# Kernel optimization log

Hardware: AMD Instinct MI355X
Metric: run time of the kernel (lower is better)

The kernel has to match this reference:

```python
import jax, jax.numpy as jnp
import numpy as np

H = 16      # n_head
DK = 64     # d_k = n_feat // n_head
EPS = 1e-5  # nn.LayerNorm default eps


def _layernorm(x, gamma, beta):
    # LayerNorm over the last (d_k) dim, matching nn.LayerNorm(d_k)
    mu = jnp.mean(x, axis=-1, keepdims=True)
    var = jnp.mean(jnp.square(x - mu), axis=-1, keepdims=True)
    return (x - mu) * jax.lax.rsqrt(var + EPS) * gamma + beta


def setup_inputs() -> dict:
    key = jax.random.key(0)
    ks = jax.random.split(key, 10)
    B, T, D = 4, 1024, 1024
    s = 0.02
    inp = {
        "query": jax.random.normal(ks[0], (B, T, D), dtype=jnp.float32),
        "key":   jax.random.normal(ks[1], (B, T, D), dtype=jnp.float32),
        "value": jax.random.normal(ks[2], (B, T, D), dtype=jnp.float32),
        "mask":  jax.random.randint(ks[3], (B, T, T), 0, 2).astype(bool),
        # projection weights (torch nn.Linear: y = x @ W.T + b)
        "Wq": jax.random.normal(ks[4], (D, D), dtype=jnp.float32) * s,
        "bq": jnp.zeros((D,), dtype=jnp.float32),
        "Wk": jax.random.normal(ks[5], (D, D), dtype=jnp.float32) * s,
        "bk": jnp.zeros((D,), dtype=jnp.float32),
        "Wv": jax.random.normal(ks[6], (D, D), dtype=jnp.float32) * s,
        "bv": jnp.zeros((D,), dtype=jnp.float32),
        "Wo": jax.random.normal(ks[7], (D, D), dtype=jnp.float32) * s,
        "bo": jnp.zeros((D,), dtype=jnp.float32),
        # per-head LayerNorm params over d_k
        "q_gamma": jnp.ones((DK,), dtype=jnp.float32),
        "q_beta":  jnp.zeros((DK,), dtype=jnp.float32),
        "k_gamma": jnp.ones((DK,), dtype=jnp.float32),
        "k_beta":  jnp.zeros((DK,), dtype=jnp.float32),
    }
    return inp


def reference(query, key, value, mask, Wq, bq, Wk, bk, Wv, bv, Wo, bo,
              q_gamma, q_beta, k_gamma, k_beta):
    B, Tq, D = query.shape
    Tk = key.shape[1]
    # forward_qkv: project, split heads, QK-LayerNorm
    q = (query @ Wq.T + bq).reshape(B, Tq, H, DK)
    k = (key   @ Wk.T + bk).reshape(B, Tk, H, DK)
    q = _layernorm(q, q_gamma, q_beta).transpose(0, 2, 1, 3)  # (B,H,Tq,dk)
    k = _layernorm(k, k_gamma, k_beta).transpose(0, 2, 1, 3)  # (B,H,Tk,dk)
    v = (value @ Wv.T + bv).reshape(B, Tk, H, DK).transpose(0, 2, 1, 3)
    # scores scaled by sqrt(d_k)
    scores = jnp.einsum('bhqd,bhkd->bhqk', q, k) / jnp.sqrt(jnp.float32(DK))
    m = mask[:, None]  # (B,1,Tq,Tk) broadcast over heads
    scores = jnp.where(m, jnp.float32(-10000.0), scores)
    attn = jax.nn.softmax(scores, axis=-1)
    attn = jnp.where(m, jnp.float32(0.0), attn)
    # dropout is identity (p=0.0, eval)
    x = jnp.einsum('bhqk,bhkd->bhqd', attn, v)
    x = x.transpose(0, 2, 1, 3).reshape(B, Tq, H * DK)
    return x @ Wo.T + bo
```

## Files before the change

### kernel.cpp

```cpp
#include <hip/hip_runtime.h>
#include <cstdint>
#include <cstddef>

typedef _Float16 half8  __attribute__((ext_vector_type(8)));
typedef _Float16 half4v __attribute__((ext_vector_type(4)));
typedef float    f32x4  __attribute__((ext_vector_type(4)));

__device__ __forceinline__ f32x4 fzero4() {
  f32x4 v; v[0] = v[1] = v[2] = v[3] = 0.0f; return v;
}

__device__ __forceinline__ void gload16(const void* g, void* l) {
  __builtin_amdgcn_global_load_lds(
      (const __attribute__((address_space(1))) unsigned int*)g,
      (__attribute__((address_space(3))) unsigned int*)l, 16, 0, 0);
}

#define MFMA(a, b, c) __builtin_amdgcn_mfma_f32_16x16x32_f16(a, b, c, 0, 0, 0)
#define EXP2(x) __builtin_amdgcn_exp2f(x)

__device__ __forceinline__ float row16_sum(float x) {
#define STEP_(N)                                                         \
  {                                                                      \
    int t_ = __builtin_amdgcn_update_dpp(0, __float_as_int(x), 0x120 | N, \
                                         0xf, 0xf, true);                \
    x = x + __int_as_float(t_);                                          \
  }
  STEP_(8) STEP_(4) STEP_(2) STEP_(1)
#undef STEP_
  return x;
}

struct PrepArgs {
  const float* src[7];
  _Float16*    dst[7];
  const int*   mask;
  unsigned long long* mbits;
};

__global__ __launch_bounds__(256) void prep_kernel(PrepArgs a) {
  const int z = blockIdx.y;
  const int nthr = gridDim.x * blockDim.x;
  const int t0 = blockIdx.x * blockDim.x + threadIdx.x;
  if (z < 3) {
    const float4* __restrict__ s = (const float4*)a.src[z];
    half4v* __restrict__ d = (half4v*)a.dst[z];
    float4 v[8];
#pragma unroll
    for (int k = 0; k < 8; ++k) v[k] = s[t0 + k * nthr];
#pragma unroll
    for (int k = 0; k < 8; ++k) {
      half4v h;
      h[0] = (_Float16)v[k].x; h[1] = (_Float16)v[k].y;
      h[2] = (_Float16)v[k].z; h[3] = (_Float16)v[k].w;
      d[t0 + k * nthr] = h;
    }
  } else if (z < 7) {
    const float4* __restrict__ s = (const float4*)a.src[z];
    half4v* __restrict__ d = (half4v*)a.dst[z];
    float4 v[2];
#pragma unroll
    for (int k = 0; k < 2; ++k) v[k] = s[t0 + k * nthr];
#pragma unroll
    for (int k = 0; k < 2; ++k) {
      half4v h;
      h[0] = (_Float16)v[k].x; h[1] = (_Float16)v[k].y;
      h[2] = (_Float16)v[k].z; h[3] = (_Float16)v[k].w;
      d[t0 + k * nthr] = h;
    }
  } else {
    const int* __restrict__ src = a.mask;
    const unsigned char* __restrict__ s8 = (const unsigned char*)src;
    unsigned long long* __restrict__ dst = a.mbits;
    const int lane = threadIdx.x & 63;
    unsigned probe = 0;
#pragma unroll
    for (int e = 0; e < 16; ++e) probe |= s8[4 * (lane * 16 + e) + 1];
    const bool isbool = __any(probe != 0);

    const int gw = blockIdx.x * 4 + (threadIdx.x >> 6);
    for (int ii = 0; ii < 32; ii += 8) {
      int mv[8];
#pragma unroll
      for (int k = 0; k < 8; ++k) {
        const int word = gw * 32 + ii + k;
        const int t = word & 1023;
        const int kw = (word >> 10) & 15;
        const int b = word >> 14;
        const size_t idx = ((size_t)(b * 1024 + t)) * 1024 + kw * 64 + lane;
        mv[k] = isbool ? (int)s8[idx] : src[idx];
      }
#pragma unroll
      for (int k = 0; k < 8; ++k) {
        unsigned long long bal = __ballot(mv[k] != 0);
        if (lane == 0) dst[gw * 32 + ii + k] = bal;
      }
    }
  }
}

#define SM_SCALE 0.18033688011112042f

__global__ __launch_bounds__(256) void proj_kernel(
    const _Float16* __restrict__ q16, const _Float16* __restrict__ k16,
    const _Float16* __restrict__ v16, const _Float16* __restrict__ w16,
    const float* __restrict__ bq, const float* __restrict__ bk,
    const float* __restrict__ bv,
    const float* __restrict__ qg, const float* __restrict__ qbt,
    const float* __restrict__ kg, const float* __restrict__ kbt,
    _Float16* __restrict__ Qln, _Float16* __restrict__ Kln,
    _Float16* __restrict__ VT) {
  __shared__ _Float16 As[2][128 * 64];
  __shared__ _Float16 Bs[2][128 * 64];

  const int tid = threadIdx.x;
  const int w = tid >> 6, lane = tid & 63, g = lane >> 4, l15 = lane & 15;
  const int flat = blockIdx.x;
  const int swz = (flat & 7) * 96 + (flat >> 3);
  const int bn = swz & 7;
  const int bm = (swz >> 3) & 31;
  const int z = swz >> 8;

  const _Float16* A = (z == 0) ? q16 : ((z == 1) ? k16 : v16);
  const _Float16* W = w16 + (size_t)z * (1024 * 1024);
  const float* bias = (z == 0) ? bq : ((z == 1) ? bk : bv);

  const int wr = w >> 1, wc = w & 1;
  const int srow = (w << 3) + (lane >> 3);
  const int csw = ((lane & 7) ^ (lane >> 3)) << 3;
  const int rsw = (l15 & 7) << 3;

  f32x4 acc[4][4];
#pragma unroll
  for (int i = 0; i < 4; ++i)
#pragma unroll
    for (int j = 0; j < 4; ++j) acc[i][j] = fzero4();

#define PROJ_STAGE(KT, BUF)                                                 \
  _Pragma("unroll") for (int r = 0; r < 4; ++r) {                           \
    const int row = r * 32 + srow;                                          \
    gload16(A + (size_t)(bm * 128 + row) * 1024 + (KT)*64 + csw,            \
            &As[BUF][(r * 32 + (w << 3)) * 64]);                            \
    gload16(W + (size_t)(bn * 128 + row) * 1024 + (KT)*64 + csw,            \
            &Bs[BUF][(r * 32 + (w << 3)) * 64]);                            \
  }

#define PROJ_TILE(KT, CUR, NXT, PF)                                         \
  {                                                                         \
    if (PF) { PROJ_STAGE((KT) + 1, NXT) }                                   \
    _Pragma("unroll") for (int kk = 0; kk < 2; ++kk) {                      \
      half8 a[4], b[4];                                                     \
      _Pragma("unroll") for (int mi = 0; mi < 4; ++mi) a[mi] =              \
          *(const half8*)&As[CUR][(wr * 64 + mi * 16 + l15) * 64 +          \
                                  ((kk * 32 + g * 8) ^ rsw)];               \
      _Pragma("unroll") for (int nj = 0; nj < 4; ++nj) b[nj] =              \
          *(const half8*)&Bs[CUR][(wc * 64 + nj * 16 + l15) * 64 +          \
                                  ((kk * 32 + g * 8) ^ rsw)];               \
      __builtin_amdgcn_s_setprio(1);                                        \
      _Pragma("unroll") for (int mi = 0; mi < 4; ++mi)                      \
          _Pragma("unroll") for (int nj = 0; nj < 4; ++nj) acc[mi][nj] =    \
              MFMA(a[mi], b[nj], acc[mi][nj]);                              \
      __builtin_amdgcn_s_setprio(0);                                        \
    }                                                                       \
    if (PF) {                                                               \
      asm volatile("s_waitcnt vmcnt(0)" ::: "memory");                      \
      __syncthreads();                                                      \
    }                                                                       \
  }

  PROJ_STAGE(0, 0)
  asm volatile("s_waitcnt vmcnt(0)" ::: "memory");
  __syncthreads();
  for (int kt = 0; kt < 16; kt += 2) {
    PROJ_TILE(kt, 0, 1, true);
    PROJ_TILE(kt + 1, 1, 0, (kt + 1) < 15);
  }
#undef PROJ_TILE
#undef PROJ_STAGE

  const int colbase = bn * 128 + wc * 64;
  const int h = colbase >> 6;
  const int rowbase = bm * 128 + wr * 64;

  float biasv[4];
#pragma unroll
  for (int nj = 0; nj < 4; ++nj) biasv[nj] = bias[colbase + nj * 16 + l15];

  if (z < 2) {
    const float* gamma = (z == 0) ? qg : kg;
    const float* beta = (z == 0) ? qbt : kbt;
    const float sc = (z == 0) ? SM_SCALE : 1.0f;
    _Float16* dst = (z == 0) ? Qln : Kln;
    float gam[4], bet[4];
#pragma unroll
    for (int nj = 0; nj < 4; ++nj) {
      gam[nj] = gamma[nj * 16 + l15] * sc;
      bet[nj] = beta[nj * 16 + l15] * sc;
    }
#pragma unroll
    for (int mi = 0; mi < 4; ++mi) {
#pragma unroll
      for (int j = 0; j < 4; ++j) {
        float vals[4], s = 0.f, s2 = 0.f;
#pragma unroll
        for (int nj = 0; nj < 4; ++nj) {
          float v = acc[mi][nj][j] + biasv[nj];
          vals[nj] = v; s += v; s2 += v * v;
        }
        s = row16_sum(s);
        s2 = row16_sum(s2);
        const float mu = s * (1.0f / 64.0f);
        const float var = s2 * (1.0f / 64.0f) - mu * mu;
        const float rs = rsqrtf(var + 1e-5f);
        const int r = rowbase + mi * 16 + g * 4 + j;
        const int b = r >> 10, t = r & 1023;
        _Float16* drow = dst + ((size_t)((b * 16 + h) * 1024 + t)) * 64;
#pragma unroll
        for (int nj = 0; nj < 4; ++nj)
          drow[nj * 16 + l15] =
              (_Float16)((vals[nj] - mu) * rs * gam[nj] + bet[nj]);
      }
    }
  } else {
#pragma unroll
    for (int mi = 0; mi < 4; ++mi) {
      const int r0 = rowbase + mi * 16 + g * 4;
      const int b = r0 >> 10, t0 = r0 & 1023;
#pragma unroll
      for (int nj = 0; nj < 4; ++nj) {
        const int dk = nj * 16 + l15;
        half4v pk;
#pragma unroll
        for (int j = 0; j < 4; ++j)
          pk[j] = (_Float16)(acc[mi][nj][j] + biasv[nj]);
        *(half4v*)&VT[((size_t)((b * 16 + h) * 64 + dk)) * 1024 + t0] = pk;
      }
    }
  }
}

#define PSTR 76

__global__ __launch_bounds__(512) void attn_kernel(
    const _Float16* __restrict__ Qln, const _Float16* __restrict__ Kln,
    const _Float16* __restrict__ VT,
    const unsigned long long* __restrict__ mbits, _Float16* __restrict__ X) {
  __shared__ _Float16 PQ[128 * PSTR];
  __shared__ _Float16 Ks[2][64 * 64];
  __shared__ _Float16 Vs[2][64 * 64];
  __shared__ unsigned long long Mb[2][128];

  const int tid = threadIdx.x;
  const int w = tid >> 6, lane = tid & 63, g = lane >> 4, l15 = lane & 15;
  const int qt = blockIdx.y;
  const int bh = blockIdx.x;
  const int b = bh >> 4, h = bh & 15;

  const int lr8 = lane >> 3;
  const int csw = ((lane & 7) ^ lr8) << 3;

  const _Float16* Qb = Qln + (size_t)bh * 65536;
  const _Float16* Kb = Kln + (size_t)bh * 65536;
  const _Float16* Vb = VT + (size_t)bh * 65536;
  const unsigned long long* mbb = mbits + (size_t)b * 16384 + qt * 128;

  gload16(Qb + (size_t)(qt * 128 + w * 16 + lr8) * 64 + csw, &PQ[(w * 16) * 64]);
  gload16(Qb + (size_t)(qt * 128 + w * 16 + 8 + lr8) * 64 + csw,
          &PQ[(w * 16 + 8) * 64]);
  gload16(Kb + (size_t)(w * 8 + lr8) * 64 + csw, &Ks[0][(w * 8) * 64]);
  gload16(Vb + (size_t)(w * 8 + lr8) * 1024 + csw, &Vs[0][(w * 8) * 64]);
  if (w == 0) gload16(mbb + lane * 2, &Mb[0][0]);
  asm volatile("s_waitcnt vmcnt(0)" ::: "memory");
  __syncthreads();

  const int rsw = (l15 & 7) << 3;
  half8 qf[2];
#pragma unroll
  for (int kk = 0; kk < 2; ++kk)
    qf[kk] = *(const half8*)&PQ[(w * 16 + l15) * 64 + ((kk * 32 + g * 8) ^ rsw)];
  asm volatile("s_waitcnt lgkmcnt(0)" ::: "memory");
  __syncthreads();

  f32x4 o[4];
  float lsum[4];
#pragma unroll
  for (int dn = 0; dn < 4; ++dn) o[dn] = fzero4();
#pragma unroll
  for (int j = 0; j < 4; ++j) lsum[j] = 0.f;

#define ATTN_TILE(KT, CUR, NXT, PF)                                          \
  {                                                                          \
    if (PF) {                                                                \
      gload16(Kb + (size_t)(((KT) + 1) * 64 + w * 8 + lr8) * 64 + csw,       \
              &Ks[NXT][(w * 8) * 64]);                                       \
      gload16(Vb + (size_t)(w * 8 + lr8) * 1024 + ((KT) + 1) * 64 + csw,     \
              &Vs[NXT][(w * 8) * 64]);                                       \
      if (w == 0)                                                            \
        gload16(mbb + (size_t)((KT) + 1) * 1024 + lane * 2, &Mb[NXT][0]);    \
    }                                                                        \
    f32x4 s[4];                                                              \
    _Pragma("unroll") for (int nj = 0; nj < 4; ++nj) s[nj] = fzero4();       \
    _Pragma("unroll") for (int kk = 0; kk < 2; ++kk) {                       \
      half8 qv = qf[kk];                                                     \
      __builtin_amdgcn_s_setprio(1);                                         \
      _Pragma("unroll") for (int nj = 0; nj < 4; ++nj) {                     \
        half8 kf = *(const half8*)&Ks[CUR][(nj * 16 + l15) * 64 +            \
                                          ((kk * 32 + g * 8) ^ rsw)];        \
        s[nj] = MFMA(qv, kf, s[nj]);                                         \
      }                                                                      \
      __builtin_amdgcn_s_setprio(0);                                         \
    }                                                                        \
    _Pragma("unroll") for (int j = 0; j < 4; ++j) {                          \
      const int lrow = w * 16 + g * 4 + j;                                   \
      const unsigned long long mw = Mb[CUR][lrow];                           \
      const unsigned lo = (unsigned)mw, hi = (unsigned)(mw >> 32);           \
      const float p0 = ((lo >> l15) & 1) ? 0.f : EXP2(s[0][j]);              \
      const float p1 = ((lo >> (l15 + 16)) & 1) ? 0.f : EXP2(s[1][j]);       \
      const float p2 = ((hi >> l15) & 1) ? 0.f : EXP2(s[2][j]);              \
      const float p3 = ((hi >> (l15 + 16)) & 1) ? 0.f : EXP2(s[3][j]);       \
      PQ[lrow * PSTR + 0 + l15] = (_Float16)p0;                              \
      PQ[lrow * PSTR + 16 + l15] = (_Float16)p1;                             \
      PQ[lrow * PSTR + 32 + l15] = (_Float16)p2;                             \
      PQ[lrow * PSTR + 48 + l15] = (_Float16)p3;                             \
      lsum[j] += (p0 + p1) + (p2 + p3);                                      \
    }                                                                        \
    _Pragma("unroll") for (int kk = 0; kk < 2; ++kk) {                       \
      half8 pa = *(const half8*)&PQ[(w * 16 + l15) * PSTR + kk * 32 + g * 8];\
      __builtin_amdgcn_s_setprio(1);                                         \
      _Pragma("unroll") for (int dn = 0; dn < 4; ++dn) {                     \
        half8 vf = *(const half8*)&Vs[CUR][(dn * 16 + l15) * 64 +            \
                                           ((kk * 32 + g * 8) ^ rsw)];       \
        o[dn] = MFMA(pa, vf, o[dn]);                                         \
      }                                                                      \
      __builtin_amdgcn_s_setprio(0);                                         \
    }                                                                        \
    if (PF) {                                                                \
      asm volatile("s_waitcnt vmcnt(0)" ::: "memory");                       \
      __syncthreads();                                                       \
    }                                                                        \
  }

  for (int kt = 0; kt < 16; kt += 2) {
    ATTN_TILE(kt, 0, 1, true);
    ATTN_TILE(kt + 1, 1, 0, (kt + 1) < 15);
  }
#undef ATTN_TILE

#pragma unroll
  for (int j = 0; j < 4; ++j) {
    const int t = qt * 128 + w * 16 + g * 4 + j;
    const float inv = 1.0f / row16_sum(lsum[j]);
    _Float16* xrow = X + ((size_t)(b * 1024 + t)) * 1024 + h * 64;
#pragma unroll
    for (int dn = 0; dn < 4; ++dn)
      xrow[dn * 16 + l15] = (_Float16)(o[dn][j] * inv);
  }
}

__global__ __launch_bounds__(256) void ogemm_kernel(
    const _Float16* __restrict__ Xin, const _Float16* __restrict__ Wo16,
    const float* __restrict__ bo, float* __restrict__ out) {
  __shared__ _Float16 As[2][128 * 64];
  __shared__ _Float16 Bs[2][64 * 64];

  const int tid = threadIdx.x;
  const int w = tid >> 6, lane = tid & 63, g = lane >> 4, l15 = lane & 15;
  const int flat = blockIdx.x;
  const int swz = (flat & 7) * 64 + (flat >> 3);
  const int bn = swz & 15;
  const int bm = swz >> 4;
  const int wr = w >> 1, wc = w & 1;
  const int srow = (w << 3) + (lane >> 3);
  const int lr8 = lane >> 3;
  const int csw = ((lane & 7) ^ lr8) << 3;
  const int rsw = (l15 & 7) << 3;

  f32x4 acc[4][2];
#pragma unroll
  for (int i = 0; i < 4; ++i)
#pragma unroll
    for (int j = 0; j < 2; ++j) acc[i][j] = fzero4();

#define OG_STAGE(KT, BUF)                                                   \
  {                                                                         \
    _Pragma("unroll") for (int r = 0; r < 4; ++r) {                         \
      gload16(Xin + (size_t)(bm * 128 + r * 32 + srow) * 1024 + (KT)*64 +   \
                  csw,                                                      \
              &As[BUF][(r * 32 + (w << 3)) * 64]);                          \
    }                                                                       \
    _Pragma("unroll") for (int c = 0; c < 2; ++c) {                         \
      gload16(Wo16 + (size_t)(bn * 64 + w * 16 + c * 8 + lr8) * 1024 +      \
                  (KT)*64 + csw,                                            \
              &Bs[BUF][(w * 16 + c * 8) * 64]);                             \
    }                                                                       \
  }

#define OG_TILE(KT, CUR, NXT, PF)                                           \
  {                                                                         \
    if (PF) { OG_STAGE((KT) + 1, NXT) }                                     \
    _Pragma("unroll") for (int kk = 0; kk < 2; ++kk) {                      \
      half8 a[4], b[2];                                                     \
      _Pragma("unroll") for (int mi = 0; mi < 4; ++mi) a[mi] =              \
          *(const half8*)&As[CUR][(wr * 64 + mi * 16 + l15) * 64 +          \
                                  ((kk * 32 + g * 8) ^ rsw)];               \
      _Pragma("unroll") for (int nj = 0; nj < 2; ++nj) b[nj] =              \
          *(const half8*)&Bs[CUR][(wc * 32 + nj * 16 + l15) * 64 +          \
                                  ((kk * 32 + g * 8) ^ rsw)];               \
      __builtin_amdgcn_s_setprio(1);                                        \
      _Pragma("unroll") for (int mi = 0; mi < 4; ++mi)                      \
          _Pragma("unroll") for (int nj = 0; nj < 2; ++nj) acc[mi][nj] =    \
              MFMA(a[mi], b[nj], acc[mi][nj]);                              \
      __builtin_amdgcn_s_setprio(0);                                        \
    }                                                                       \
    if (PF) {                                                               \
      asm volatile("s_waitcnt vmcnt(0)" ::: "memory");                      \
      __syncthreads();                                                      \
    }                                                                       \
  }

  OG_STAGE(0, 0)
  asm volatile("s_waitcnt vmcnt(0)" ::: "memory");
  __syncthreads();
  for (int kt = 0; kt < 16; kt += 2) {
    OG_TILE(kt, 0, 1, true);
    OG_TILE(kt + 1, 1, 0, (kt + 1) < 15);
  }
#undef OG_TILE
#undef OG_STAGE

  const int colbase = bn * 64 + wc * 32;
  const int rowbase = bm * 128 + wr * 64;
  float biasv[2];
#pragma unroll
  for (int nj = 0; nj < 2; ++nj) biasv[nj] = bo[colbase + nj * 16 + l15];
#pragma unroll
  for (int mi = 0; mi < 4; ++mi)
#pragma unroll
    for (int nj = 0; nj < 2; ++nj)
#pragma unroll
      for (int j = 0; j < 4; ++j) {
        const int r = rowbase + mi * 16 + g * 4 + j;
        out[(size_t)r * 1024 + colbase + nj * 16 + l15] =
            acc[mi][nj][j] + biasv[nj];
      }
}

extern "C" void kernel_launch(void* const* d_in, const int* in_sizes, int n_in,
                              void* d_out, int out_size, void* d_ws,
                              size_t ws_size, hipStream_t stream) {
  const float* query = (const float*)d_in[0];
  const float* key = (const float*)d_in[1];
  const float* value = (const float*)d_in[2];
  const int* mask = (const int*)d_in[3];
  const float* Wq = (const float*)d_in[4];
  const float* bq = (const float*)d_in[5];
  const float* Wk = (const float*)d_in[6];
  const float* bk = (const float*)d_in[7];
  const float* Wv = (const float*)d_in[8];
  const float* bv = (const float*)d_in[9];
  const float* Wo = (const float*)d_in[10];
  const float* bo = (const float*)d_in[11];
  const float* qg = (const float*)d_in[12];
  const float* qb = (const float*)d_in[13];
  const float* kg = (const float*)d_in[14];
  const float* kb = (const float*)d_in[15];
  float* out = (float*)d_out;

  const size_t M4 = (size_t)4 * 1024 * 1024;
  const size_t M1 = (size_t)1024 * 1024;
  _Float16* q16 = (_Float16*)d_ws;
  _Float16* k16 = q16 + M4;
  _Float16* v16 = k16 + M4;
  _Float16* w16 = v16 + M4;
  _Float16* Qln = w16 + M4;
  _Float16* Kln = Qln + M4;
  _Float16* VTp = Kln + M4;
  _Float16* X = q16;
  unsigned long long* mbits = (unsigned long long*)(VTp + M4);

  PrepArgs pa;
  pa.src[0] = query; pa.src[1] = key; pa.src[2] = value;
  pa.src[3] = Wq; pa.src[4] = Wk; pa.src[5] = Wv; pa.src[6] = Wo;
  pa.dst[0] = q16; pa.dst[1] = k16; pa.dst[2] = v16;
  pa.dst[3] = w16; pa.dst[4] = w16 + M1; pa.dst[5] = w16 + 2 * M1;
  pa.dst[6] = w16 + 3 * M1;
  pa.mask = mask;
  pa.mbits = mbits;

  prep_kernel<<<dim3(512, 8), 256, 0, stream>>>(pa);
  proj_kernel<<<dim3(768), 256, 0, stream>>>(
      q16, k16, v16, w16, bq, bk, bv, qg, qb, kg, kb, Qln, Kln, VTp);
  attn_kernel<<<dim3(64, 8), 512, 0, stream>>>(Qln, Kln, VTp, mbits, X);
  ogemm_kernel<<<dim3(512), 256, 0, stream>>>(X, w16 + 3 * M1, bo, out);
}
```

Baseline: 120.2 us.

## Fuse fp32-to-fp16 activation conversion into projection GEMM A-tile loading

```diff
diff --git a/kernel.cpp b/kernel.cpp
--- a/kernel.cpp
+++ b/kernel.cpp
@@ -32,8 +32,8 @@
 }
 
 struct PrepArgs {
-  const float* src[7];
-  _Float16*    dst[7];
+  const float* wsrc[4];
+  _Float16*    wdst[4];
   const int*   mask;
   unsigned long long* mbits;
 };
@@ -42,22 +42,9 @@
   const int z = blockIdx.y;
   const int nthr = gridDim.x * blockDim.x;
   const int t0 = blockIdx.x * blockDim.x + threadIdx.x;
-  if (z < 3) {
-    const float4* __restrict__ s = (const float4*)a.src[z];
-    half4v* __restrict__ d = (half4v*)a.dst[z];
-    float4 v[8];
-#pragma unroll
-    for (int k = 0; k < 8; ++k) v[k] = s[t0 + k * nthr];
-#pragma unroll
-    for (int k = 0; k < 8; ++k) {
-      half4v h;
-      h[0] = (_Float16)v[k].x; h[1] = (_Float16)v[k].y;
-      h[2] = (_Float16)v[k].z; h[3] = (_Float16)v[k].w;
-      d[t0 + k * nthr] = h;
-    }
-  } else if (z < 7) {
-    const float4* __restrict__ s = (const float4*)a.src[z];
-    half4v* __restrict__ d = (half4v*)a.dst[z];
+  if (z < 4) {
+    const float4* __restrict__ s = (const float4*)a.wsrc[z];
+    half4v* __restrict__ d = (half4v*)a.wdst[z];
     float4 v[2];
 #pragma unroll
     for (int k = 0; k < 2; ++k) v[k] = s[t0 + k * nthr];
@@ -102,8 +89,8 @@
 #define SM_SCALE 0.18033688011112042f
 
 __global__ __launch_bounds__(256) void proj_kernel(
-    const _Float16* __restrict__ q16, const _Float16* __restrict__ k16,
-    const _Float16* __restrict__ v16, const _Float16* __restrict__ w16,
+    const float* __restrict__ query, const float* __restrict__ key,
+    const float* __restrict__ value, const _Float16* __restrict__ w16,
     const float* __restrict__ bq, const float* __restrict__ bk,
     const float* __restrict__ bv,
     const float* __restrict__ qg, const float* __restrict__ qbt,
@@ -121,7 +108,7 @@
   const int bm = (swz >> 3) & 31;
   const int z = swz >> 8;
 
-  const _Float16* A = (z == 0) ? q16 : ((z == 1) ? k16 : v16);
+  const float* Af = (z == 0) ? query : ((z == 1) ? key : value);
   const _Float16* W = w16 + (size_t)z * (1024 * 1024);
   const float* bias = (z == 0) ? bq : ((z == 1) ? bk : bv);
 
@@ -130,24 +117,45 @@
   const int csw = ((lane & 7) ^ (lane >> 3)) << 3;
   const int rsw = (l15 & 7) << 3;
 
+  const int arow0 = tid >> 3;
+  const int acg = tid & 7;
+  const int axor = ((acg ^ (arow0 & 7)) << 3);
+
   f32x4 acc[4][4];
 #pragma unroll
   for (int i = 0; i < 4; ++i)
 #pragma unroll
     for (int j = 0; j < 4; ++j) acc[i][j] = fzero4();
 
-#define PROJ_STAGE(KT, BUF)                                                 \
+  float4 va[4][2];
+
+#define PROJ_LOADA(KT)                                                      \
+  _Pragma("unroll") for (int s_ = 0; s_ < 4; ++s_) {                        \
+    const float4* ap_ = (const float4*)(Af +                                \
+        (size_t)(bm * 128 + s_ * 32 + arow0) * 1024 + (KT)*64 + acg * 8);   \
+    va[s_][0] = ap_[0];                                                     \
+    va[s_][1] = ap_[1];                                                     \
+  }
+
+#define PROJ_WRITEA(BUF)                                                    \
+  _Pragma("unroll") for (int s_ = 0; s_ < 4; ++s_) {                        \
+    half8 h_;                                                               \
+    h_[0] = (_Float16)va[s_][0].x; h_[1] = (_Float16)va[s_][0].y;           \
+    h_[2] = (_Float16)va[s_][0].z; h_[3] = (_Float16)va[s_][0].w;           \
+    h_[4] = (_Float16)va[s_][1].x; h_[5] = (_Float16)va[s_][1].y;           \
+    h_[6] = (_Float16)va[s_][1].z; h_[7] = (_Float16)va[s_][1].w;           \
+    *(half8*)&As[BUF][(s_ * 32 + arow0) * 64 + axor] = h_;                  \
+  }
+
+#define PROJ_STAGEB(KT, BUF)                                                \
   _Pragma("unroll") for (int r = 0; r < 4; ++r) {                           \
-    const int row = r * 32 + srow;                                          \
-    gload16(A + (size_t)(bm * 128 + row) * 1024 + (KT)*64 + csw,            \
-            &As[BUF][(r * 32 + (w << 3)) * 64]);                            \
-    gload16(W + (size_t)(bn * 128 + row) * 1024 + (KT)*64 + csw,            \
+    gload16(W + (size_t)(bn * 128 + r * 32 + srow) * 1024 + (KT)*64 + csw,  \
             &Bs[BUF][(r * 32 + (w << 3)) * 64]);                            \
   }
 
 #define PROJ_TILE(KT, CUR, NXT, PF)                                         \
   {                                                                         \
-    if (PF) { PROJ_STAGE((KT) + 1, NXT) }                                   \
+    if (PF) { PROJ_LOADA((KT) + 1) PROJ_STAGEB((KT) + 1, NXT) }             \
     _Pragma("unroll") for (int kk = 0; kk < 2; ++kk) {                      \
       half8 a[4], b[4];                                                     \
       _Pragma("unroll") for (int mi = 0; mi < 4; ++mi) a[mi] =              \
@@ -164,19 +172,24 @@
     }                                                                       \
     if (PF) {                                                               \
       asm volatile("s_waitcnt vmcnt(0)" ::: "memory");                      \
+      PROJ_WRITEA(NXT)                                                      \
       __syncthreads();                                                      \
     }                                                                       \
   }
 
-  PROJ_STAGE(0, 0)
+  PROJ_LOADA(0)
+  PROJ_STAGEB(0, 0)
   asm volatile("s_waitcnt vmcnt(0)" ::: "memory");
+  PROJ_WRITEA(0)
   __syncthreads();
   for (int kt = 0; kt < 16; kt += 2) {
     PROJ_TILE(kt, 0, 1, true);
     PROJ_TILE(kt + 1, 1, 0, (kt + 1) < 15);
   }
 #undef PROJ_TILE
-#undef PROJ_STAGE
+#undef PROJ_STAGEB
+#undef PROJ_WRITEA
+#undef PROJ_LOADA
 
   const int colbase = bn * 128 + wc * 64;
   const int h = colbase >> 6;
@@ -468,28 +481,24 @@
 
   const size_t M4 = (size_t)4 * 1024 * 1024;
   const size_t M1 = (size_t)1024 * 1024;
-  _Float16* q16 = (_Float16*)d_ws;
-  _Float16* k16 = q16 + M4;
-  _Float16* v16 = k16 + M4;
-  _Float16* w16 = v16 + M4;
-  _Float16* Qln = w16 + M4;
-  _Float16* Kln = Qln + M4;
-  _Float16* VTp = Kln + M4;
-  _Float16* X = q16;
-  unsigned long long* mbits = (unsigned long long*)(VTp + M4);
+  _Float16* base = (_Float16*)d_ws;
+  _Float16* X = base;
+  _Float16* w16 = base + 3 * M4;
+  _Float16* Qln = base + 4 * M4;
+  _Float16* Kln = base + 5 * M4;
+  _Float16* VTp = base + 6 * M4;
+  unsigned long long* mbits = (unsigned long long*)(base + 7 * M4);
 
   PrepArgs pa;
-  pa.src[0] = query; pa.src[1] = key; pa.src[2] = value;
-  pa.src[3] = Wq; pa.src[4] = Wk; pa.src[5] = Wv; pa.src[6] = Wo;
-  pa.dst[0] = q16; pa.dst[1] = k16; pa.dst[2] = v16;
-  pa.dst[3] = w16; pa.dst[4] = w16 + M1; pa.dst[5] = w16 + 2 * M1;
-  pa.dst[6] = w16 + 3 * M1;
+  pa.wsrc[0] = Wq; pa.wsrc[1] = Wk; pa.wsrc[2] = Wv; pa.wsrc[3] = Wo;
+  pa.wdst[0] = w16; pa.wdst[1] = w16 + M1; pa.wdst[2] = w16 + 2 * M1;
+  pa.wdst[3] = w16 + 3 * M1;
   pa.mask = mask;
   pa.mbits = mbits;
 
-  prep_kernel<<<dim3(512, 8), 256, 0, stream>>>(pa);
+  prep_kernel<<<dim3(512, 5), 256, 0, stream>>>(pa);
   proj_kernel<<<dim3(768), 256, 0, stream>>>(
-      q16, k16, v16, w16, bq, bk, bv, qg, qb, kg, kb, Qln, Kln, VTp);
+      query, key, value, w16, bq, bk, bv, qg, qb, kg, kb, Qln, Kln, VTp);
   attn_kernel<<<dim3(64, 8), 512, 0, stream>>>(Qln, Kln, VTp, mbits, X);
   ogemm_kernel<<<dim3(512), 256, 0, stream>>>(X, w16 + 3 * M1, bo, out);
 }
```

Result: no change. 119.5 us (-0.6%).
